# Performance work log

Hardware: AMD Instinct MI355X
Metric: run time of the kernel (lower is better)

Reference implementation:

```python
import jax, jax.numpy as jnp
import numpy as np

ALPHA, GAMMA = 0.25, 2.0
THR = 0.85            # soft_target_threshold
KL_EPS = 1e-6
FOCAL_EPS = 1e-8
VOC = 96              # len(vocab); index VOC is blank/pad


def setup_inputs() -> dict:
    key = jax.random.key(0)
    ks = jax.random.split(key, 6)
    bs, nq, n_pts, num_gt, L = 16, 200, 25, 32, 25
    return {
        "pred_logits": jax.random.normal(ks[0], (bs, nq, n_pts, 1), jnp.float32),
        "pred_ctrl_points": jax.random.uniform(ks[1], (bs, nq, n_pts, 2), jnp.float32),
        "pred_text_logits": jax.random.normal(ks[2], (bs, nq, n_pts, VOC + 1), jnp.float32),
        "tgt_ctrl_points": jax.random.uniform(ks[3], (bs, num_gt, n_pts, 2), jnp.float32),
        "tgt_texts": jax.random.randint(ks[4], (bs, num_gt, L), 0, VOC + 1),
        "centroids": jax.random.normal(ks[5], (VOC, 256), jnp.float32),
    }


def _cost_matrix(pred_logits, pred_ctrl_points, pred_text_logits,
                 tgt_ctrl_points, tgt_texts, centroids):
    bs, nq, n_pts, _ = pred_logits.shape
    num_gt = tgt_texts.shape[1]

    # ---- focal classification cost (mean over control points) ----
    out_prob = jax.nn.sigmoid(pred_logits.reshape(bs * nq, n_pts, -1))
    neg = (1.0 - ALPHA) * out_prob ** GAMMA * (-jnp.log1p(-(out_prob - FOCAL_EPS)))
    neg = (1.0 - ALPHA) * out_prob ** GAMMA * (-jnp.log(1.0 - out_prob + FOCAL_EPS))
    pos = ALPHA * (1.0 - out_prob) ** GAMMA * (-jnp.log(out_prob + FOCAL_EPS))
    cost_class = (pos[..., 0] - neg[..., 0]).mean(-1, keepdims=True)  # [bs*nq, 1]

    # ---- L1 cdist over flattened control points ----
    out_pts = pred_ctrl_points.reshape(bs * nq, n_pts * 2)
    tgt_pts = tgt_ctrl_points.reshape(bs * num_gt, n_pts * 2)
    cost_kpts = jnp.abs(out_pts[:, None, :] - tgt_pts[None, :, :]).sum(-1)  # [bs*nq, bs*num_gt]

    # ---- linguistic KL-div cost (per-batch block diagonal) ----
    probs = jax.nn.softmax(pred_text_logits, axis=-1)          # [bs,nq,n_pts,VOC+1]
    pred_avg = probs[..., :VOC].mean(axis=2)                   # [bs,nq,VOC]
    P = pred_avg + KL_EPS
    P = P / P.sum(-1, keepdims=True)
    logP = jnp.log(P)

    # soft target distribution per character (generate_soft_target_sequence)
    cn = centroids / jnp.linalg.norm(centroids, axis=-1, keepdims=True)
    soft_all = THR * jnp.eye(VOC, dtype=P.dtype) + (1.0 - THR) * jax.nn.softmax(cn @ cn.T, axis=-1)  # [VOC,VOC]

    mask = (tgt_texts != VOC)                                  # [bs,num_gt,L]
    lengths = mask.sum(-1)                                     # [bs,num_gt]
    per_char = soft_all[jnp.clip(tgt_texts, 0, VOC - 1)]       # [bs,num_gt,L,VOC]
    tgt_avg = (per_char * mask[..., None]).sum(2) / jnp.maximum(lengths, 1)[..., None].astype(P.dtype)
    T = tgt_avg + KL_EPS
    T = T / T.sum(-1, keepdims=True)                           # [bs,num_gt,VOC]

    # KL(T || P) = sum T*logT - sum T*logP, vectorized over (query, gt)
    kl = (T * jnp.log(T)).sum(-1)[:, None, :] - jnp.einsum('bqv,bgv->bqg', logP, T)  # [bs,nq,num_gt]
    kl = jnp.where(lengths[:, None, :] == 0, 100.0, kl)

    # place per-batch blocks on the diagonal of the global cost matrix
    eye = jnp.eye(bs, dtype=kl.dtype)
    cost_text = jnp.einsum('bqg,bc->bqcg', kl, eye).reshape(bs * nq, bs * num_gt)

    C = 1.0 * cost_class + 1.0 * cost_kpts + 1.0 * cost_text   # class/coord/text weights = 1
    return C.reshape(bs, nq, bs * num_gt)


def reference(pred_logits, pred_ctrl_points, pred_text_logits,
              tgt_ctrl_points, tgt_texts, centroids):
    return _cost_matrix(pred_logits, pred_ctrl_points, pred_text_logits,
                        tgt_ctrl_points, tgt_texts, centroids)
```

## Files before the change

kernel.cpp:

```cpp
#include <hip/hip_runtime.h>
#include <hip/hip_bf16.h>

#define BS 16
#define NQ 200
#define NPTS 25
#define VOC 96
#define VOCP1 97
#define NGT 32
#define LSEQ 25
#define NCOL (BS*NGT)
#define NBQ (BS*NQ)
#define KL_EPS 1e-6f
#define FOCAL_EPS 1e-8f

__global__ __launch_bounds__(128) void k1_pred(
        const float* __restrict__ pred_logits,
        const float* __restrict__ pred_text_logits,
        float* __restrict__ logP,
        float* __restrict__ cost_class)
{
    const int bq   = blockIdx.x;
    const int tid  = threadIdx.x;
    const int wave = tid >> 6, lane = tid & 63;
    __shared__ float s_exp[NPTS * VOCP1];
    __shared__ float s_invden[NPTS];
    __shared__ float s_part[2];

    const float* tl = pred_text_logits + (size_t)bq * NPTS * VOCP1;
    for (int i = tid; i < NPTS * VOCP1; i += 128)
        s_exp[i] = __expf(tl[i]);
    __syncthreads();

    const int grp = tid >> 5, sub = tid & 31;
    for (int p0 = 0; p0 < NPTS; p0 += 4) {
        int p = p0 + grp;
        float s = 0.f;
        if (p < NPTS)
            for (int v = sub; v < VOCP1; v += 32) s += s_exp[p * VOCP1 + v];
        #pragma unroll
        for (int off = 16; off; off >>= 1) s += __shfl_xor(s, off);
        if (p < NPTS && sub == 0) s_invden[p] = 1.0f / s;
    }

    if (wave == 0) {
        float cc = 0.f;
        if (lane < NPTS) {
            float x = pred_logits[bq * NPTS + lane];
            float p = 1.f / (1.f + __expf(-x));
            float pos = 0.25f * (1.f - p) * (1.f - p) * (-__logf(p + FOCAL_EPS));
            float neg = 0.75f * p * p * (-__logf(1.f - p + FOCAL_EPS));
            cc = pos - neg;
        }
        #pragma unroll
        for (int off = 32; off; off >>= 1) cc += __shfl_xor(cc, off);
        if (lane == 0) cost_class[bq] = cc * (1.0f / NPTS);
    }
    __syncthreads();

    float avg = 0.f;
    if (tid < VOC) {
        float a = 0.f;
        #pragma unroll
        for (int p = 0; p < NPTS; p++)
            a += s_exp[p * VOCP1 + tid] * s_invden[p];
        avg = a * (1.0f / NPTS);
    }
    float s = avg;
    #pragma unroll
    for (int off = 32; off; off >>= 1) s += __shfl_xor(s, off);
    if (lane == 0) s_part[wave] = s;
    __syncthreads();
    float denom = s_part[0] + s_part[1] + (float)VOC * KL_EPS;
    if (tid < VOC)
        logP[(size_t)bq * VOC + tid] = __logf((avg + KL_EPS) / denom);
}

__global__ __launch_bounds__(128) void k2a_soft(
        const float* __restrict__ centroids,
        float* __restrict__ soft)
{
    const int i   = blockIdx.x;
    const int tid = threadIdx.x;
    const int wave = tid >> 6, lane = tid & 63;
    __shared__ float row[256];
    __shared__ float s_part[2];
    for (int k = tid; k < 64; k += 128)
        *(float4*)&row[k * 4] = *(const float4*)&centroids[i * 256 + k * 4];
    __syncthreads();

    float e = 0.f;
    if (tid < VOC) {
        float dij = 0.f, djj = 0.f, dii = 0.f;
        const float4* cj = (const float4*)(centroids + (size_t)tid * 256);
        #pragma unroll 4
        for (int k = 0; k < 64; k++) {
            float4 b = cj[k];
            float4 a = *(const float4*)&row[k * 4];
            dij += a.x * b.x + a.y * b.y + a.z * b.z + a.w * b.w;
            djj += b.x * b.x + b.y * b.y + b.z * b.z + b.w * b.w;
            dii += a.x * a.x + a.y * a.y + a.z * a.z + a.w * a.w;
        }
        float sim = dij * rsqrtf(dii * djj);
        e = __expf(sim);
    }
    float s = e;
    #pragma unroll
    for (int off = 32; off; off >>= 1) s += __shfl_xor(s, off);
    if (lane == 0) s_part[wave] = s;
    __syncthreads();
    float den = s_part[0] + s_part[1];
    if (tid < VOC) {
        float v = 0.15f * e / den;
        if (tid == i) v += 0.85f;
        soft[i * VOC + tid] = v;
    }
}

__global__ __launch_bounds__(128) void k2b_T(
        const int* __restrict__ tgt_texts,
        const float* __restrict__ soft,
        float* __restrict__ T,
        float* __restrict__ TlogT,
        int* __restrict__ lens)
{
    const int bg   = blockIdx.x;
    const int tid  = threadIdx.x;
    const int wave = tid >> 6, lane = tid & 63;
    __shared__ float s_part[2];
    __shared__ int   s_chars[LSEQ];
    __shared__ int   s_len;

    if (tid < LSEQ) s_chars[tid] = tgt_texts[bg * LSEQ + tid];
    __syncthreads();
    if (wave == 0) {
        int t = (lane < LSEQ) ? s_chars[lane] : VOC;
        unsigned long long m = __ballot(t != VOC);
        if (lane == 0) s_len = __popcll(m);
    }
    __syncthreads();
    const int len = s_len;

    float avg = 0.f;
    if (tid < VOC) {
        float a = 0.f;
        for (int l = 0; l < LSEQ; l++) {
            int t = s_chars[l];
            if (t != VOC) a += soft[t * VOC + tid];
        }
        avg = a / (float)(len > 0 ? len : 1);
    }
    float s = avg;
    #pragma unroll
    for (int off = 32; off; off >>= 1) s += __shfl_xor(s, off);
    if (lane == 0) s_part[wave] = s;
    __syncthreads();
    float denom = s_part[0] + s_part[1] + (float)VOC * KL_EPS;
    float t = (avg + KL_EPS) / denom;
    float tl = 0.f;
    if (tid < VOC) {
        T[(size_t)bg * VOC + tid] = t;
        tl = t * __logf(t);
    }
    __syncthreads();
    float s2 = tl;
    #pragma unroll
    for (int off = 32; off; off >>= 1) s2 += __shfl_xor(s2, off);
    if (lane == 0) s_part[wave] = s2;
    __syncthreads();
    if (tid == 0) {
        TlogT[bg] = s_part[0] + s_part[1];
        lens[bg]  = len;
    }
}

#define K3_ROWS 25
#define K3_COLS 256
__global__ __launch_bounds__(256) void k3_cost(
        const float* __restrict__ pred_ctrl,
        const float* __restrict__ tgt_ctrl,
        const float* __restrict__ logP,
        const float* __restrict__ cost_class,
        const float* __restrict__ T,
        const float* __restrict__ TlogT,
        const int* __restrict__ lens,
        float* __restrict__ out)
{
    const int rt   = blockIdx.x >> 1;
    const int ch   = blockIdx.x & 1;
    const int row0 = rt * K3_ROWS;
    const int c0   = ch * K3_COLS;
    const int b    = rt >> 3;
    const int tid  = threadIdx.x;
    const int col  = c0 + tid;

    __shared__ float s_pred[K3_ROWS][52];
    __shared__ float s_logP[K3_ROWS][VOC];
    __shared__ float s_T[NGT][VOCP1];
    __shared__ float s_text[K3_ROWS][33];
    __shared__ float s_cc[K3_ROWS];

    const bool has_text = ((b < 8) == (ch == 0));
    const int  jb0 = b * NGT - c0;

    const float* pg = pred_ctrl + (size_t)row0 * 50;
    for (int i = tid; i < K3_ROWS * 50; i += 256) {
        int r = i / 50, d = i - r * 50;
        s_pred[r][d] = pg[i];
    }
    if (tid < K3_ROWS) s_cc[tid] = cost_class[row0 + tid];
    if (has_text) {
        for (int i = tid; i < K3_ROWS * VOC; i += 256) {
            int r = i / VOC, v = i - r * VOC;
            s_logP[r][v] = logP[(size_t)(row0 + r) * VOC + v];
        }
        for (int i = tid; i < NGT * VOC; i += 256) {
            int g = i / VOC, v = i - g * VOC;
            s_T[g][v] = T[(size_t)(b * NGT + g) * VOC + v];
        }
    }

    float tg[50];
    {
        const float2* trow = (const float2*)(tgt_ctrl + (size_t)col * 50);
        #pragma unroll
        for (int q = 0; q < 25; q++) {
            float2 v = trow[q];
            tg[2 * q] = v.x; tg[2 * q + 1] = v.y;
        }
    }
    __syncthreads();

    if (has_text) {
        for (int i = tid; i < K3_ROWS * NGT; i += 256) {
            int r = i >> 5, g = i & 31;
            int c = b * NGT + g;
            float txt;
            if (lens[c] == 0) {
                txt = 100.f;
            } else {
                float d0 = 0.f, d1 = 0.f;
                #pragma unroll
                for (int v = 0; v < VOC; v += 2) {
                    d0 += s_logP[r][v]     * s_T[g][v];
                    d1 += s_logP[r][v + 1] * s_T[g][v + 1];
                }
                txt = TlogT[c] - (d0 + d1);
            }
            s_text[r][g] = txt;
        }
        __syncthreads();
    }

    for (int r = 0; r < K3_ROWS; r++) {
        float kp0 = 0.f, kp1 = 0.f, kp2 = 0.f, kp3 = 0.f;
        #pragma unroll
        for (int q = 0; q < 12; q++) {
            float4 p = *(const float4*)&s_pred[r][q * 4];
            kp0 += fabsf(p.x - tg[q * 4 + 0]);
            kp1 += fabsf(p.y - tg[q * 4 + 1]);
            kp2 += fabsf(p.z - tg[q * 4 + 2]);
            kp3 += fabsf(p.w - tg[q * 4 + 3]);
        }
        kp0 += fabsf(s_pred[r][48] - tg[48]);
        kp1 += fabsf(s_pred[r][49] - tg[49]);
        float val = s_cc[r] + (kp0 + kp1) + (kp2 + kp3);
        if (has_text) {
            unsigned g = (unsigned)(tid - jb0);
            if (g < (unsigned)NGT) val += s_text[r][g];
        }
        out[(size_t)(row0 + r) * NCOL + col] = val;
    }
}

extern "C" void kernel_launch(void* const* d_in, const int* in_sizes, int n_in,
                              void* d_out, int out_size, void* d_ws, size_t ws_size,
                              hipStream_t stream) {
    const float* pred_logits = (const float*)d_in[0];
    const float* pred_ctrl   = (const float*)d_in[1];
    const float* pred_text   = (const float*)d_in[2];
    const float* tgt_ctrl    = (const float*)d_in[3];
    const int*   tgt_texts   = (const int*)d_in[4];
    const float* centroids   = (const float*)d_in[5];
    float* out = (float*)d_out;

    float* ws        = (float*)d_ws;
    float* logP      = ws;
    float* costclass = logP + (size_t)NBQ * VOC;
    float* soft      = costclass + NBQ;
    float* T         = soft + VOC * VOC;
    float* TlogT     = T + (size_t)NCOL * VOC;
    int*   lens      = (int*)(TlogT + NCOL);

    k1_pred<<<NBQ, 128, 0, stream>>>(pred_logits, pred_text, logP, costclass);
    k2a_soft<<<VOC, 128, 0, stream>>>(centroids, soft);
    k2b_T<<<NCOL, 128, 0, stream>>>(tgt_texts, soft, T, TlogT, lens);
    k3_cost<<<256, 256, 0, stream>>>(pred_ctrl, tgt_ctrl, logP, costclass,
                                     T, TlogT, lens, out);
}
```

Measured before the change: 132.0 us.

## Merge pred and soft-target kernels; compute target distributions inside cost kernel

```diff
diff --git a/kernel.cpp b/kernel.cpp
--- a/kernel.cpp
+++ b/kernel.cpp
@@ -13,215 +13,152 @@
 #define KL_EPS 1e-6f
 #define FOCAL_EPS 1e-8f
 
-__global__ __launch_bounds__(128) void k1_pred(
+__global__ __launch_bounds__(128) void kA(
         const float* __restrict__ pred_logits,
         const float* __restrict__ pred_text_logits,
+        const float* __restrict__ centroids,
         float* __restrict__ logP,
-        float* __restrict__ cost_class)
+        float* __restrict__ cost_class,
+        float* __restrict__ soft)
 {
-    const int bq   = blockIdx.x;
     const int tid  = threadIdx.x;
     const int wave = tid >> 6, lane = tid & 63;
-    __shared__ float s_exp[NPTS * VOCP1];
+    __shared__ float s_buf[NPTS * VOCP1];
     __shared__ float s_invden[NPTS];
     __shared__ float s_part[2];
 
-    const float* tl = pred_text_logits + (size_t)bq * NPTS * VOCP1;
-    for (int i = tid; i < NPTS * VOCP1; i += 128)
-        s_exp[i] = __expf(tl[i]);
-    __syncthreads();
-
-    const int grp = tid >> 5, sub = tid & 31;
-    for (int p0 = 0; p0 < NPTS; p0 += 4) {
-        int p = p0 + grp;
-        float s = 0.f;
-        if (p < NPTS)
-            for (int v = sub; v < VOCP1; v += 32) s += s_exp[p * VOCP1 + v];
-        #pragma unroll
-        for (int off = 16; off; off >>= 1) s += __shfl_xor(s, off);
-        if (p < NPTS && sub == 0) s_invden[p] = 1.0f / s;
-    }
-
-    if (wave == 0) {
-        float cc = 0.f;
-        if (lane < NPTS) {
-            float x = pred_logits[bq * NPTS + lane];
-            float p = 1.f / (1.f + __expf(-x));
-            float pos = 0.25f * (1.f - p) * (1.f - p) * (-__logf(p + FOCAL_EPS));
-            float neg = 0.75f * p * p * (-__logf(1.f - p + FOCAL_EPS));
-            cc = pos - neg;
-        }
-        #pragma unroll
-        for (int off = 32; off; off >>= 1) cc += __shfl_xor(cc, off);
-        if (lane == 0) cost_class[bq] = cc * (1.0f / NPTS);
-    }
-    __syncthreads();
-
-    float avg = 0.f;
-    if (tid < VOC) {
-        float a = 0.f;
-        #pragma unroll
-        for (int p = 0; p < NPTS; p++)
-            a += s_exp[p * VOCP1 + tid] * s_invden[p];
-        avg = a * (1.0f / NPTS);
-    }
-    float s = avg;
-    #pragma unroll
-    for (int off = 32; off; off >>= 1) s += __shfl_xor(s, off);
-    if (lane == 0) s_part[wave] = s;
-    __syncthreads();
-    float denom = s_part[0] + s_part[1] + (float)VOC * KL_EPS;
-    if (tid < VOC)
-        logP[(size_t)bq * VOC + tid] = __logf((avg + KL_EPS) / denom);
+    if (blockIdx.x < NBQ) {
+        const int bq = blockIdx.x;
+        const float* tl = pred_text_logits + (size_t)bq * NPTS * VOCP1;
+        for (int i = tid; i < NPTS * VOCP1; i += 128)
+            s_buf[i] = __expf(tl[i]);
+        __syncthreads();
+
+        const int grp = tid >> 5, sub = tid & 31;
+        for (int p0 = 0; p0 < NPTS; p0 += 4) {
+            int p = p0 + grp;
+            float s = 0.f;
+            if (p < NPTS)
+                for (int v = sub; v < VOCP1; v += 32) s += s_buf[p * VOCP1 + v];
+            #pragma unroll
+            for (int off = 16; off; off >>= 1) s += __shfl_xor(s, off, 32);
+            if (p < NPTS && sub == 0) s_invden[p] = 1.0f / s;
+        }
+
+        if (wave == 0) {
+            float cc = 0.f;
+            if (lane < NPTS) {
+                float x = pred_logits[bq * NPTS + lane];
+                float p = 1.f / (1.f + __expf(-x));
+                float pos = 0.25f * (1.f - p) * (1.f - p) * (-__logf(p + FOCAL_EPS));
+                float neg = 0.75f * p * p * (-__logf(1.f - p + FOCAL_EPS));
+                cc = pos - neg;
+            }
+            #pragma unroll
+            for (int off = 32; off; off >>= 1) cc += __shfl_xor(cc, off);
+            if (lane == 0) cost_class[bq] = cc * (1.0f / NPTS);
+        }
+        __syncthreads();
+
+        float avg = 0.f;
+        if (tid < VOC) {
+            float a = 0.f;
+            #pragma unroll
+            for (int p = 0; p < NPTS; p++)
+                a += s_buf[p * VOCP1 + tid] * s_invden[p];
+            avg = a * (1.0f / NPTS);
+        }
+        float s = avg;
+        #pragma unroll
+        for (int off = 32; off; off >>= 1) s += __shfl_xor(s, off);
+        if (lane == 0) s_part[wave] = s;
+        __syncthreads();
+        float denom = s_part[0] + s_part[1] + (float)VOC * KL_EPS;
+        if (tid < VOC)
+            logP[(size_t)bq * VOC + tid] = __logf((avg + KL_EPS) / denom);
+    } else {
+        const int i = blockIdx.x - NBQ;
+        for (int k = tid; k < 64; k += 128)
+            *(float4*)&s_buf[k * 4] = *(const float4*)&centroids[i * 256 + k * 4];
+        __syncthreads();
+
+        float e = 0.f;
+        if (tid < VOC) {
+            float dij = 0.f, djj = 0.f, dii = 0.f;
+            const float4* cj = (const float4*)(centroids + (size_t)tid * 256);
+            #pragma unroll 4
+            for (int k = 0; k < 64; k++) {
+                float4 b = cj[k];
+                float4 a = *(const float4*)&s_buf[k * 4];
+                dij += a.x * b.x + a.y * b.y + a.z * b.z + a.w * b.w;
+                djj += b.x * b.x + b.y * b.y + b.z * b.z + b.w * b.w;
+                dii += a.x * a.x + a.y * a.y + a.z * a.z + a.w * a.w;
+            }
+            float sim = dij * rsqrtf(dii * djj);
+            e = __expf(sim);
+        }
+        float s = e;
+        #pragma unroll
+        for (int off = 32; off; off >>= 1) s += __shfl_xor(s, off);
+        if (lane == 0) s_part[wave] = s;
+        __syncthreads();
+        float den = s_part[0] + s_part[1];
+        if (tid < VOC) {
+            float v = 0.15f * e / den;
+            if (tid == i) v += 0.85f;
+            soft[i * VOC + tid] = v;
+        }
+    }
 }
 
-__global__ __launch_bounds__(128) void k2a_soft(
-        const float* __restrict__ centroids,
-        float* __restrict__ soft)
-{
-    const int i   = blockIdx.x;
-    const int tid = threadIdx.x;
-    const int wave = tid >> 6, lane = tid & 63;
-    __shared__ float row[256];
-    __shared__ float s_part[2];
-    for (int k = tid; k < 64; k += 128)
-        *(float4*)&row[k * 4] = *(const float4*)&centroids[i * 256 + k * 4];
-    __syncthreads();
-
-    float e = 0.f;
-    if (tid < VOC) {
-        float dij = 0.f, djj = 0.f, dii = 0.f;
-        const float4* cj = (const float4*)(centroids + (size_t)tid * 256);
-        #pragma unroll 4
-        for (int k = 0; k < 64; k++) {
-            float4 b = cj[k];
-            float4 a = *(const float4*)&row[k * 4];
-            dij += a.x * b.x + a.y * b.y + a.z * b.z + a.w * b.w;
-            djj += b.x * b.x + b.y * b.y + b.z * b.z + b.w * b.w;
-            dii += a.x * a.x + a.y * a.y + a.z * a.z + a.w * a.w;
-        }
-        float sim = dij * rsqrtf(dii * djj);
-        e = __expf(sim);
-    }
-    float s = e;
-    #pragma unroll
-    for (int off = 32; off; off >>= 1) s += __shfl_xor(s, off);
-    if (lane == 0) s_part[wave] = s;
-    __syncthreads();
-    float den = s_part[0] + s_part[1];
-    if (tid < VOC) {
-        float v = 0.15f * e / den;
-        if (tid == i) v += 0.85f;
-        soft[i * VOC + tid] = v;
-    }
-}
-
-__global__ __launch_bounds__(128) void k2b_T(
-        const int* __restrict__ tgt_texts,
-        const float* __restrict__ soft,
-        float* __restrict__ T,
-        float* __restrict__ TlogT,
-        int* __restrict__ lens)
-{
-    const int bg   = blockIdx.x;
-    const int tid  = threadIdx.x;
-    const int wave = tid >> 6, lane = tid & 63;
-    __shared__ float s_part[2];
-    __shared__ int   s_chars[LSEQ];
-    __shared__ int   s_len;
-
-    if (tid < LSEQ) s_chars[tid] = tgt_texts[bg * LSEQ + tid];
-    __syncthreads();
-    if (wave == 0) {
-        int t = (lane < LSEQ) ? s_chars[lane] : VOC;
-        unsigned long long m = __ballot(t != VOC);
-        if (lane == 0) s_len = __popcll(m);
-    }
-    __syncthreads();
-    const int len = s_len;
-
-    float avg = 0.f;
-    if (tid < VOC) {
-        float a = 0.f;
-        for (int l = 0; l < LSEQ; l++) {
-            int t = s_chars[l];
-            if (t != VOC) a += soft[t * VOC + tid];
-        }
-        avg = a / (float)(len > 0 ? len : 1);
-    }
-    float s = avg;
-    #pragma unroll
-    for (int off = 32; off; off >>= 1) s += __shfl_xor(s, off);
-    if (lane == 0) s_part[wave] = s;
-    __syncthreads();
-    float denom = s_part[0] + s_part[1] + (float)VOC * KL_EPS;
-    float t = (avg + KL_EPS) / denom;
-    float tl = 0.f;
-    if (tid < VOC) {
-        T[(size_t)bg * VOC + tid] = t;
-        tl = t * __logf(t);
-    }
-    __syncthreads();
-    float s2 = tl;
-    #pragma unroll
-    for (int off = 32; off; off >>= 1) s2 += __shfl_xor(s2, off);
-    if (lane == 0) s_part[wave] = s2;
-    __syncthreads();
-    if (tid == 0) {
-        TlogT[bg] = s_part[0] + s_part[1];
-        lens[bg]  = len;
-    }
-}
-
-#define K3_ROWS 25
-#define K3_COLS 256
-__global__ __launch_bounds__(256) void k3_cost(
+__global__ __launch_bounds__(256) void kC(
         const float* __restrict__ pred_ctrl,
         const float* __restrict__ tgt_ctrl,
         const float* __restrict__ logP,
         const float* __restrict__ cost_class,
-        const float* __restrict__ T,
-        const float* __restrict__ TlogT,
-        const int* __restrict__ lens,
+        const float* __restrict__ soft,
+        const int* __restrict__ tgt_texts,
         float* __restrict__ out)
 {
     const int rt   = blockIdx.x >> 1;
     const int ch   = blockIdx.x & 1;
-    const int row0 = rt * K3_ROWS;
-    const int c0   = ch * K3_COLS;
+    const int row0 = rt * NPTS;
+    const int c0   = ch * 256;
     const int b    = rt >> 3;
     const int tid  = threadIdx.x;
-    const int col  = c0 + tid;
-
-    __shared__ float s_pred[K3_ROWS][52];
-    __shared__ float s_logP[K3_ROWS][VOC];
+
+    __shared__ float s_pred[NPTS][52];
+    __shared__ float s_logP[NPTS][VOC];
     __shared__ float s_T[NGT][VOCP1];
-    __shared__ float s_text[K3_ROWS][33];
-    __shared__ float s_cc[K3_ROWS];
+    __shared__ float s_text[NPTS][NGT + 1];
+    __shared__ float s_cc[NPTS];
+    __shared__ int   s_chars[NGT][LSEQ];
+    __shared__ float s_TlogT[NGT];
+    __shared__ int   s_len[NGT];
 
     const bool has_text = ((b < 8) == (ch == 0));
     const int  jb0 = b * NGT - c0;
 
     const float* pg = pred_ctrl + (size_t)row0 * 50;
-    for (int i = tid; i < K3_ROWS * 50; i += 256) {
-        int r = i / 50, d = i - r * 50;
-        s_pred[r][d] = pg[i];
-    }
-    if (tid < K3_ROWS) s_cc[tid] = cost_class[row0 + tid];
+    for (int i = tid; i < NPTS * 50; i += 256) {
+        int r = i / 50;
+        s_pred[r][i - r * 50] = pg[i];
+    }
+    if (tid < NPTS) s_cc[tid] = cost_class[row0 + tid];
     if (has_text) {
-        for (int i = tid; i < K3_ROWS * VOC; i += 256) {
+        for (int i = tid; i < NPTS * VOC; i += 256) {
             int r = i / VOC, v = i - r * VOC;
             s_logP[r][v] = logP[(size_t)(row0 + r) * VOC + v];
         }
-        for (int i = tid; i < NGT * VOC; i += 256) {
-            int g = i / VOC, v = i - g * VOC;
-            s_T[g][v] = T[(size_t)(b * NGT + g) * VOC + v];
+        for (int i = tid; i < NGT * LSEQ; i += 256) {
+            int g = i / LSEQ, l = i - g * LSEQ;
+            s_chars[g][l] = tgt_texts[(b * NGT + g) * LSEQ + l];
         }
     }
 
     float tg[50];
     {
-        const float2* trow = (const float2*)(tgt_ctrl + (size_t)col * 50);
+        const float2* trow = (const float2*)(tgt_ctrl + (size_t)(c0 + tid) * 50);
         #pragma unroll
         for (int q = 0; q < 25; q++) {
             float2 v = trow[q];
@@ -231,11 +168,39 @@
     __syncthreads();
 
     if (has_text) {
-        for (int i = tid; i < K3_ROWS * NGT; i += 256) {
+        const int grp = tid >> 5, sub = tid & 31;
+        for (int g = grp; g < NGT; g += 8) {
+            int len = 0;
+            float a0 = 0.f, a1 = 0.f, a2 = 0.f;
+            for (int l = 0; l < LSEQ; l++) {
+                int t = s_chars[g][l];
+                if (t != VOC) {
+                    len++;
+                    const float* sr = soft + t * VOC;
+                    a0 += sr[sub]; a1 += sr[sub + 32]; a2 += sr[sub + 64];
+                }
+            }
+            float inv = 1.f / (float)(len > 0 ? len : 1);
+            a0 *= inv; a1 *= inv; a2 *= inv;
+            float s = a0 + a1 + a2;
+            #pragma unroll
+            for (int off = 16; off; off >>= 1) s += __shfl_xor(s, off, 32);
+            float denom = s + (float)VOC * KL_EPS;
+            float t0 = (a0 + KL_EPS) / denom;
+            float t1 = (a1 + KL_EPS) / denom;
+            float t2 = (a2 + KL_EPS) / denom;
+            s_T[g][sub] = t0; s_T[g][sub + 32] = t1; s_T[g][sub + 64] = t2;
+            float tl = t0 * __logf(t0) + t1 * __logf(t1) + t2 * __logf(t2);
+            #pragma unroll
+            for (int off = 16; off; off >>= 1) tl += __shfl_xor(tl, off, 32);
+            if (sub == 0) { s_TlogT[g] = tl; s_len[g] = len; }
+        }
+        __syncthreads();
+
+        for (int i = tid; i < NPTS * NGT; i += 256) {
             int r = i >> 5, g = i & 31;
-            int c = b * NGT + g;
             float txt;
-            if (lens[c] == 0) {
+            if (s_len[g] == 0) {
                 txt = 100.f;
             } else {
                 float d0 = 0.f, d1 = 0.f;
@@ -244,14 +209,14 @@
                     d0 += s_logP[r][v]     * s_T[g][v];
                     d1 += s_logP[r][v + 1] * s_T[g][v + 1];
                 }
-                txt = TlogT[c] - (d0 + d1);
+                txt = s_TlogT[g] - (d0 + d1);
             }
             s_text[r][g] = txt;
         }
         __syncthreads();
     }
 
-    for (int r = 0; r < K3_ROWS; r++) {
+    for (int r = 0; r < NPTS; r++) {
         float kp0 = 0.f, kp1 = 0.f, kp2 = 0.f, kp3 = 0.f;
         #pragma unroll
         for (int q = 0; q < 12; q++) {
@@ -265,10 +230,10 @@
         kp1 += fabsf(s_pred[r][49] - tg[49]);
         float val = s_cc[r] + (kp0 + kp1) + (kp2 + kp3);
         if (has_text) {
-            unsigned g = (unsigned)(tid - jb0);
+            unsigned g = (unsigned)((int)tid - jb0);
             if (g < (unsigned)NGT) val += s_text[r][g];
         }
-        out[(size_t)(row0 + r) * NCOL + col] = val;
+        out[(size_t)(row0 + r) * NCOL + (c0 + tid)] = val;
     }
 }
 
@@ -287,13 +252,9 @@
     float* logP      = ws;
     float* costclass = logP + (size_t)NBQ * VOC;
     float* soft      = costclass + NBQ;
-    float* T         = soft + VOC * VOC;
-    float* TlogT     = T + (size_t)NCOL * VOC;
-    int*   lens      = (int*)(TlogT + NCOL);
-
-    k1_pred<<<NBQ, 128, 0, stream>>>(pred_logits, pred_text, logP, costclass);
-    k2a_soft<<<VOC, 128, 0, stream>>>(centroids, soft);
-    k2b_T<<<NCOL, 128, 0, stream>>>(tgt_texts, soft, T, TlogT, lens);
-    k3_cost<<<256, 256, 0, stream>>>(pred_ctrl, tgt_ctrl, logP, costclass,
-                                     T, TlogT, lens, out);
+
+    kA<<<NBQ + VOC, 128, 0, stream>>>(pred_logits, pred_text, centroids,
+                                      logP, costclass, soft);
+    kC<<<256, 256, 0, stream>>>(pred_ctrl, tgt_ctrl, logP, costclass,
+                                soft, tgt_texts, out);
 }
```

Result: no change. 132.3 us (+0.2%).
